# Performance work log

Hardware: AMD Instinct MI355X
Metric: run time of the kernel (lower is better)

## Reference

```python
import jax, jax.numpy as jnp
import numpy as np

IN_F, RED, WID, CLS, T = 700, 256, 4096, 20, 100


def _q4(W):
    # per-tensor symmetric INT4 STE: value is quantized, grad is identity
    scale = jnp.maximum(jnp.abs(W).max() / 7.0, 1e-8)
    return W + jax.lax.stop_gradient(jnp.round(W / scale) * scale - W)


def setup_inputs() -> dict:
    key = jax.random.key(0)
    ks = jax.random.split(key, 12)
    B = 64
    x = jax.random.normal(ks[0], (B, T, IN_F), dtype=jnp.float32)
    latent = jax.random.uniform(ks[1], (T,), dtype=jnp.float32)
    spatial_W = jax.random.normal(ks[2], (RED, IN_F), jnp.float32) / np.sqrt(IN_F)
    spatial_b = jnp.zeros((RED,), jnp.float32)
    conv_W = jax.random.normal(ks[3], (RED, RED, 5), jnp.float32) / np.sqrt(RED * 5)
    conv_b = jnp.zeros((RED,), jnp.float32)
    fc1_W = jax.random.normal(ks[4], (WID, RED), jnp.float32) / np.sqrt(RED)
    fc1_b = jnp.zeros((WID,), jnp.float32)
    fc2_W = jax.random.normal(ks[5], (CLS, WID), jnp.float32) / np.sqrt(WID)
    fc2_b = jnp.zeros((CLS,), jnp.float32)
    gain = jnp.asarray(1.0, jnp.float32)
    return {"x": x, "latent": latent, "spatial_W": spatial_W, "spatial_b": spatial_b,
            "conv_W": conv_W, "conv_b": conv_b, "fc1_W": fc1_W, "fc1_b": fc1_b,
            "fc2_W": fc2_W, "fc2_b": fc2_b, "gain": gain}


def _compute_drive(x, latent, spatial_W, spatial_b, conv_W, conv_b, fc1_W, fc1_b, gain):
    # spatial projection (INT4 STE linear) + relu : (B,T,RED)
    xp = jax.nn.relu(jnp.einsum("btf,rf->btr", x, _q4(spatial_W)) + spatial_b)
    # temporal conv1d over T, padding=2 (same), channels RED->RED
    xc = jax.lax.conv_general_dilated(
        xp.transpose(0, 2, 1), conv_W, window_strides=(1,), padding=[(2, 2)],
        dimension_numbers=("NCH", "OIH", "NCH"))
    conv_out = jax.nn.relu(xc + conv_b[None, :, None]).transpose(0, 2, 1)  # (B,T,RED)
    spatial_act = jax.nn.softplus(jnp.einsum("btr,wr->btw", conv_out, _q4(fc1_W)) + fc1_b)
    return spatial_act * latent[None, :, None] * jnp.abs(gain)  # (B,T,WID)


def reference(x, latent, spatial_W, spatial_b, conv_W, conv_b, fc1_W, fc1_b, fc2_W, fc2_b, gain):
    drive = _compute_drive(x, latent, spatial_W, spatial_b, conv_W, conv_b, fc1_W, fc1_b, gain)
    # Poisson spike sampling with straight-through estimator, then clamp at 1
    pois = jax.random.poisson(jax.random.key(42), jax.lax.stop_gradient(drive)).astype(drive.dtype)
    spikes = drive + jax.lax.stop_gradient(pois - drive)
    spikes = jnp.minimum(spikes, 1.0)
    # decay-weighted temporal reduction over T
    decay = jnp.exp(jnp.linspace(-2.0, 0.0, T)).astype(drive.dtype)
    weighted = jnp.einsum("btw,t->bw", spikes, decay)  # (B,WID)
    # dropout in eval mode = identity
    logits = weighted @ _q4(fc2_W).T + fc2_b  # (B,CLS)
    return (logits, spikes, drive)
```

## Files before the change

### kernel.cpp

```cpp
#include <hip/hip_runtime.h>
#include <stdint.h>

#define B 64
#define T 100
#define IN_F 700
#define RED 256
#define WID 4096
#define CLS 20
#define BT (B*T)
#define NELEM (BT*WID)
#define LOGITS_OFF 0
#define SPIKES_OFF (B*CLS)
#define DRIVE_OFF (SPIKES_OFF + NELEM)

#define WS_SLOTS 0
#define WS_W2Q 16
#define WS_XP  (WS_W2Q + CLS*WID)
#define WS_CO  (WS_XP + BT*RED)
#define WS_WEIGHTED (WS_CO + BT*RED)

#define SC_WST 0
#define SC_W1T (SC_WST + IN_F*RED)
#define SC_CWT (SC_W1T + RED*WID)

__host__ __device__ __forceinline__ uint32_t rotl32(uint32_t v, int r) {
  return (v << r) | (v >> (32 - r));
}

__host__ __device__ __forceinline__ void threefry2x32(uint32_t k0, uint32_t k1,
                                                      uint32_t x0, uint32_t x1,
                                                      uint32_t& o0, uint32_t& o1) {
  uint32_t k2 = k0 ^ k1 ^ 0x1BD11BDAu;
  x0 += k0; x1 += k1;
#define TF_R(r) { x0 += x1; x1 = rotl32(x1, (r)); x1 ^= x0; }
  TF_R(13) TF_R(15) TF_R(26) TF_R(6)
  x0 += k1; x1 += k2 + 1u;
  TF_R(17) TF_R(29) TF_R(16) TF_R(24)
  x0 += k2; x1 += k0 + 2u;
  TF_R(13) TF_R(15) TF_R(26) TF_R(6)
  x0 += k0; x1 += k1 + 3u;
  TF_R(17) TF_R(29) TF_R(16) TF_R(24)
  x0 += k1; x1 += k2 + 4u;
  TF_R(13) TF_R(15) TF_R(26) TF_R(6)
  x0 += k2; x1 += k0 + 5u;
#undef TF_R
  o0 = x0; o1 = x1;
}

__global__ void absmax_kernel(const float* __restrict__ w, int n, uint32_t* slot) {
  __shared__ uint32_t sm[256];
  uint32_t m = 0u;
  for (int i = blockIdx.x * 256 + threadIdx.x; i < n; i += gridDim.x * 256)
    m = max(m, __float_as_uint(fabsf(w[i])));
  sm[threadIdx.x] = m;
  __syncthreads();
  for (int s = 128; s > 0; s >>= 1) {
    if (threadIdx.x < s) sm[threadIdx.x] = max(sm[threadIdx.x], sm[threadIdx.x + s]);
    __syncthreads();
  }
  if (threadIdx.x == 0) atomicMax(slot, sm[0]);
}

__global__ void quant_t_kernel(const float* __restrict__ w, float* __restrict__ qT,
                               int Nn, int Kk, const uint32_t* __restrict__ slot) {
  float s = fmaxf(__uint_as_float(*slot) / 7.0f, 1e-8f);
  int id = blockIdx.x * 256 + threadIdx.x;
  if (id < Nn * Kk) {
    int n = id / Kk, k = id - n * Kk;
    qT[(size_t)k * Nn + n] = rintf(w[id] / s) * s;
  }
}

__global__ void quant_kernel(const float* __restrict__ w, float* __restrict__ q,
                             int n, const uint32_t* __restrict__ slot) {
  float s = fmaxf(__uint_as_float(*slot) / 7.0f, 1e-8f);
  int i = blockIdx.x * 256 + threadIdx.x;
  if (i < n) q[i] = rintf(w[i] / s) * s;
}

__global__ void convw_t_kernel(const float* __restrict__ w, float* __restrict__ wt) {
  int id = blockIdx.x * 256 + threadIdx.x;
  if (id < 256 * 1280) {
    int o = id / 1280, r = id - o * 1280;
    int ic = r / 5, h = r - ic * 5;
    wt[(size_t)((h << 8) + ic) * 256 + o] = w[id];
  }
}

template<int SRCA>
__global__ __launch_bounds__(256, 8)
void gemm32_kernel(const float* __restrict__ A, const float* __restrict__ Bt,
                   const float* __restrict__ bias, float* __restrict__ C,
                   int M, int N, int K) {
  constexpr int MT = 32, NT = 64, TM = 2, TN = 4;
  constexpr int ASR = MT + 4, BSR = NT + 4;
  __shared__ float As[32 * ASR];
  __shared__ float Bs[32 * BSR];
  int tid = threadIdx.x;
  int tx = tid & 15, ty = tid >> 4;
  int m0 = blockIdx.x * MT, n0 = blockIdx.y * NT;
  int am = tid >> 3, ak4 = (tid & 7) << 2;
  float acc[TM * TN];
#pragma unroll
  for (int i = 0; i < TM * TN; ++i) acc[i] = 0.f;

  for (int kt = 0; kt < K; kt += 32) {
    int klen = K - kt; if (klen > 32) klen = 32;
    {
      float4 av = make_float4(0.f, 0.f, 0.f, 0.f);
      if (ak4 < klen) {
        if (SRCA == 0) {
          av = *(const float4*)&A[(size_t)(m0 + am) * K + kt + ak4];
        } else {
          int k = kt + ak4;
          int h = k >> 8, ic = k & 255;
          int bt = m0 + am;
          int b = bt / T, t = bt - b * T;
          int tt = t + h - 2;
          if (tt >= 0 && tt < T)
            av = *(const float4*)&A[((size_t)(b * T + tt)) * RED + ic];
        }
      }
      As[(ak4 + 0) * ASR + am] = av.x;
      As[(ak4 + 1) * ASR + am] = av.y;
      As[(ak4 + 2) * ASR + am] = av.z;
      As[(ak4 + 3) * ASR + am] = av.w;
    }
#pragma unroll
    for (int rep = 0; rep < 2; ++rep) {
      int e = rep * 256 + tid;
      int n4 = (e & 15) << 2, kk = e >> 4;
      float4 v = make_float4(0.f, 0.f, 0.f, 0.f);
      if (kk < klen) v = *(const float4*)&Bt[(size_t)(kt + kk) * N + n0 + n4];
      *(float4*)&Bs[kk * BSR + n4] = v;
    }
    __syncthreads();
    if (klen == 32) {
#pragma unroll
      for (int kk = 0; kk < 32; ++kk) {
        float a[TM], b[TN];
#pragma unroll
        for (int i = 0; i < TM; ++i) a[i] = As[kk * ASR + ty * TM + i];
#pragma unroll
        for (int d = 0; d < TN; ++d) b[d] = Bs[kk * BSR + tx * TN + d];
#pragma unroll
        for (int j = 0; j < TM; ++j)
#pragma unroll
          for (int d = 0; d < TN; ++d)
            acc[j * TN + d] = fmaf(a[j], b[d], acc[j * TN + d]);
      }
    } else {
      for (int kk = 0; kk < klen; ++kk) {
        float a[TM], b[TN];
#pragma unroll
        for (int i = 0; i < TM; ++i) a[i] = As[kk * ASR + ty * TM + i];
#pragma unroll
        for (int d = 0; d < TN; ++d) b[d] = Bs[kk * BSR + tx * TN + d];
#pragma unroll
        for (int j = 0; j < TM; ++j)
#pragma unroll
          for (int d = 0; d < TN; ++d)
            acc[j * TN + d] = fmaf(a[j], b[d], acc[j * TN + d]);
      }
    }
    __syncthreads();
  }

  float bv[TN];
#pragma unroll
  for (int d = 0; d < TN; ++d) bv[d] = bias[n0 + tx * TN + d];
#pragma unroll
  for (int j = 0; j < TM; ++j) {
    int m = m0 + ty * TM + j;
#pragma unroll
    for (int d = 0; d < TN; ++d)
      C[(size_t)m * N + n0 + tx * TN + d] = fmaxf(acc[j * TN + d] + bv[d], 0.0f);
  }
}

__global__ __launch_bounds__(256, 4)
void fc1_kernel(const float* __restrict__ A, const float* __restrict__ Bt,
                const float* __restrict__ bias, const float* __restrict__ latent,
                const float* __restrict__ gain, float* __restrict__ C,
                int K, int N) {
  constexpr int ASR = 132, BSR = 132;
  __shared__ float As[32 * ASR];
  __shared__ float Bs[32 * BSR];
  int tid = threadIdx.x;
  int tx = tid & 15, ty = tid >> 4;
  int wid = (blockIdx.x & 7) * 200 + (blockIdx.x >> 3);
  int bx = wid % 50, by = wid / 50;
  int m0 = bx * 128, n0 = by * 128;
  float2 acc2[32];
#pragma unroll
  for (int i = 0; i < 32; ++i) acc2[i] = make_float2(0.f, 0.f);

  for (int kt = 0; kt < K; kt += 32) {
#pragma unroll
    for (int rep = 0; rep < 4; ++rep) {
      int e = rep * 256 + tid;
      int k4 = (e & 7) << 2, m = e >> 3;
      const float4 v = *(const float4*)&A[(size_t)(m0 + m) * K + kt + k4];
      As[(k4 + 0) * ASR + m] = v.x;
      As[(k4 + 1) * ASR + m] = v.y;
      As[(k4 + 2) * ASR + m] = v.z;
      As[(k4 + 3) * ASR + m] = v.w;
    }
#pragma unroll
    for (int rep = 0; rep < 4; ++rep) {
      int e = rep * 256 + tid;
      int n4 = (e & 31) << 2, kk = e >> 5;
      float4 v = *(const float4*)&Bt[(size_t)(kt + kk) * N + n0 + n4];
      *(float4*)&Bs[kk * BSR + n4] = v;
    }
    __syncthreads();
#pragma unroll
    for (int kk = 0; kk < 32; ++kk) {
      float a[8];
#pragma unroll
      for (int i = 0; i < 8; ++i) a[i] = As[kk * ASR + ty * 8 + i];
      float2 b0 = *(const float2*)&Bs[kk * BSR + tx * 4];
      float2 b1 = *(const float2*)&Bs[kk * BSR + tx * 4 + 2];
      float2 b2 = *(const float2*)&Bs[kk * BSR + 64 + tx * 4];
      float2 b3 = *(const float2*)&Bs[kk * BSR + 64 + tx * 4 + 2];
#pragma unroll
      for (int j = 0; j < 8; ++j) {
        acc2[j * 4 + 0].x = fmaf(a[j], b0.x, acc2[j * 4 + 0].x);
        acc2[j * 4 + 0].y = fmaf(a[j], b0.y, acc2[j * 4 + 0].y);
        acc2[j * 4 + 1].x = fmaf(a[j], b1.x, acc2[j * 4 + 1].x);
        acc2[j * 4 + 1].y = fmaf(a[j], b1.y, acc2[j * 4 + 1].y);
        acc2[j * 4 + 2].x = fmaf(a[j], b2.x, acc2[j * 4 + 2].x);
        acc2[j * 4 + 2].y = fmaf(a[j], b2.y, acc2[j * 4 + 2].y);
        acc2[j * 4 + 3].x = fmaf(a[j], b3.x, acc2[j * 4 + 3].x);
        acc2[j * 4 + 3].y = fmaf(a[j], b3.y, acc2[j * 4 + 3].y);
      }
    }
    __syncthreads();
  }

  float g = fabsf(gain[0]);
  float bv[8];
#pragma unroll
  for (int d = 0; d < 4; ++d) {
    bv[d] = bias[n0 + tx * 4 + d];
    bv[4 + d] = bias[n0 + 64 + tx * 4 + d];
  }
#pragma unroll
  for (int j = 0; j < 8; ++j) {
    int bt = m0 + ty * 8 + j;
    int q = bt / T;
    float lat = latent[bt - q * T];
    float o[8];
    o[0] = acc2[j * 4 + 0].x; o[1] = acc2[j * 4 + 0].y;
    o[2] = acc2[j * 4 + 1].x; o[3] = acc2[j * 4 + 1].y;
    o[4] = acc2[j * 4 + 2].x; o[5] = acc2[j * 4 + 2].y;
    o[6] = acc2[j * 4 + 3].x; o[7] = acc2[j * 4 + 3].y;
#pragma unroll
    for (int d = 0; d < 8; ++d) {
      float v = o[d] + bv[d];
      float e = expf(-fabsf(v));
      float l = log1pf(e);
      float sp = fmaxf(v, 0.0f) + l;
      o[d] = (sp * lat) * g;
    }
    float4 o0 = make_float4(o[0], o[1], o[2], o[3]);
    float4 o1 = make_float4(o[4], o[5], o[6], o[7]);
    *(float4*)&C[(size_t)bt * N + n0 + tx * 4] = o0;
    *(float4*)&C[(size_t)bt * N + n0 + 64 + tx * 4] = o1;
  }
}

__global__ __launch_bounds__(256) void spike_weighted_kernel(float* __restrict__ out,
                                                             float* __restrict__ wt,
                                                             uint32_t k0, uint32_t k1) {
  __shared__ float dec[128];
  int tid = threadIdx.x;
  if (tid < T) {
    float step = 2.0f / 99.0f;
    float a = step * (float)tid;
    dec[tid] = expf(a - 2.0f);
  }
  __syncthreads();
  int b = blockIdx.x >> 2;
  int w = ((blockIdx.x & 3) << 10) + (tid << 2);
  float acc0 = 0.f, acc1 = 0.f, acc2 = 0.f, acc3 = 0.f;
  for (int t = 0; t < T; ++t) {
    uint32_t p = (uint32_t)((b * T + t) * WID + w);
    float4 lam = *(const float4*)&out[DRIVE_OFF + p];
    float s[4];
#pragma unroll
    for (int i = 0; i < 4; ++i) {
      uint32_t y0, y1;
      threefry2x32(k0, k1, 0u, p + i, y0, y1);
      uint32_t bits = y0 ^ y1;
      float u = __uint_as_float((bits >> 9) | 0x3f800000u) - 1.0f;
      float lamv = (i == 0) ? lam.x : (i == 1) ? lam.y : (i == 2) ? lam.z : lam.w;
      s[i] = (lamv > 0.0f && logf(u) > -lamv) ? 1.0f : 0.0f;
    }
    *(float4*)&out[SPIKES_OFF + p] = make_float4(s[0], s[1], s[2], s[3]);
    float d = dec[t];
    acc0 = fmaf(s[0], d, acc0);
    acc1 = fmaf(s[1], d, acc1);
    acc2 = fmaf(s[2], d, acc2);
    acc3 = fmaf(s[3], d, acc3);
  }
  *(float4*)&wt[b * WID + w] = make_float4(acc0, acc1, acc2, acc3);
}

__global__ void logits_kernel(const float* __restrict__ wt,
                              const float* __restrict__ w2,
                              const float* __restrict__ b2,
                              float* __restrict__ out) {
  __shared__ float sm[256];
  int b = blockIdx.x / CLS, c = blockIdx.x - b * CLS;
  const float* wr = wt + (size_t)b * WID;
  const float* w2r = w2 + (size_t)c * WID;
  float p = 0.f;
  for (int w = threadIdx.x; w < WID; w += 256) p = fmaf(wr[w], w2r[w], p);
  sm[threadIdx.x] = p;
  __syncthreads();
  for (int s = 128; s > 0; s >>= 1) {
    if (threadIdx.x < s) sm[threadIdx.x] += sm[threadIdx.x + s];
    __syncthreads();
  }
  if (threadIdx.x == 0) out[LOGITS_OFF + blockIdx.x] = sm[0] + b2[c];
}

extern "C" void kernel_launch(void* const* d_in, const int* in_sizes, int n_in,
                              void* d_out, int out_size, void* d_ws, size_t ws_size,
                              hipStream_t stream) {
  (void)in_sizes; (void)n_in; (void)out_size; (void)ws_size;
  const float* x         = (const float*)d_in[0];
  const float* latent    = (const float*)d_in[1];
  const float* spatial_W = (const float*)d_in[2];
  const float* spatial_b = (const float*)d_in[3];
  const float* conv_W    = (const float*)d_in[4];
  const float* conv_b    = (const float*)d_in[5];
  const float* fc1_W     = (const float*)d_in[6];
  const float* fc1_b     = (const float*)d_in[7];
  const float* fc2_W     = (const float*)d_in[8];
  const float* fc2_b     = (const float*)d_in[9];
  const float* gain      = (const float*)d_in[10];
  float* out = (float*)d_out;
  uint32_t* wsu = (uint32_t*)d_ws;
  float* wsf = (float*)d_ws;
  float* S = out + SPIKES_OFF;

  uint32_t sk0, sk1;
  threefry2x32(0u, 42u, 0u, 1u, sk0, sk1);

  hipMemsetAsync(wsu + WS_SLOTS, 0, 3 * sizeof(uint32_t), stream);
  absmax_kernel<<<64, 256, 0, stream>>>(spatial_W, RED * IN_F, wsu + WS_SLOTS + 0);
  absmax_kernel<<<256, 256, 0, stream>>>(fc1_W, WID * RED, wsu + WS_SLOTS + 1);
  absmax_kernel<<<32, 256, 0, stream>>>(fc2_W, CLS * WID, wsu + WS_SLOTS + 2);

  quant_t_kernel<<<700, 256, 0, stream>>>(spatial_W, S + SC_WST, RED, IN_F, wsu + WS_SLOTS + 0);
  quant_t_kernel<<<4096, 256, 0, stream>>>(fc1_W, S + SC_W1T, WID, RED, wsu + WS_SLOTS + 1);
  quant_kernel<<<320, 256, 0, stream>>>(fc2_W, wsf + WS_W2Q, CLS * WID, wsu + WS_SLOTS + 2);
  convw_t_kernel<<<1280, 256, 0, stream>>>(conv_W, S + SC_CWT);

  gemm32_kernel<0><<<dim3(200, 4), 256, 0, stream>>>(
      x, S + SC_WST, spatial_b, wsf + WS_XP, BT, RED, IN_F);

  gemm32_kernel<1><<<dim3(200, 4), 256, 0, stream>>>(
      wsf + WS_XP, S + SC_CWT, conv_b, wsf + WS_CO, BT, RED, 1280);

  fc1_kernel<<<1600, 256, 0, stream>>>(
      wsf + WS_CO, S + SC_W1T, fc1_b, latent, gain, out + DRIVE_OFF, RED, WID);

  spike_weighted_kernel<<<B * 4, 256, 0, stream>>>(out, wsf + WS_WEIGHTED, sk0, sk1);

  logits_kernel<<<B * CLS, 256, 0, stream>>>(wsf + WS_WEIGHTED, wsf + WS_W2Q, fc2_b, out);
}
```

Baseline: 720.2 us.

## Double-buffer small GEMMs with 64-thread blocks and tile the weight-quantize transpose

The spatial and conv GEMMs move to a double-buffered kernel that prefetches the next K tile into registers while computing the current one. Each block now has 64 threads, each computing an 8x4 output micro-tile, and the results are stored as float4. The quantize-transpose kernel now goes through a 32x33 shared-memory tile so both its reads and its writes are coalesced. With only 64 threads per block and 800 blocks, the GEMMs may have low occupancy, and the heavier per-thread work could expose latency on this GPU.

```diff
diff --git a/kernel.cpp b/kernel.cpp
--- a/kernel.cpp
+++ b/kernel.cpp
@@ -61,13 +61,26 @@
   if (threadIdx.x == 0) atomicMax(slot, sm[0]);
 }
 
-__global__ void quant_t_kernel(const float* __restrict__ w, float* __restrict__ qT,
-                               int Nn, int Kk, const uint32_t* __restrict__ slot) {
+__global__ __launch_bounds__(256)
+void quant_t_kernel(const float* __restrict__ w, float* __restrict__ qT,
+                    int Nn, int Kk, const uint32_t* __restrict__ slot) {
+  __shared__ float tile[32][33];
   float s = fmaxf(__uint_as_float(*slot) / 7.0f, 1e-8f);
-  int id = blockIdx.x * 256 + threadIdx.x;
-  if (id < Nn * Kk) {
-    int n = id / Kk, k = id - n * Kk;
-    qT[(size_t)k * Nn + n] = rintf(w[id] / s) * s;
+  int tx = threadIdx.x & 31, ty = threadIdx.x >> 5;
+  int k0 = blockIdx.x * 32, n0 = blockIdx.y * 32;
+#pragma unroll
+  for (int r = 0; r < 32; r += 8) {
+    int n = n0 + ty + r, k = k0 + tx;
+    if (n < Nn && k < Kk) {
+      float v = w[(size_t)n * Kk + k];
+      tile[ty + r][tx] = rintf(v / s) * s;
+    }
+  }
+  __syncthreads();
+#pragma unroll
+  for (int r = 0; r < 32; r += 8) {
+    int k = k0 + ty + r, n = n0 + tx;
+    if (k < Kk && n < Nn) qT[(size_t)k * Nn + n] = tile[tx][ty + r];
   }
 }
 
@@ -88,93 +101,136 @@
 }
 
 template<int SRCA>
-__global__ __launch_bounds__(256, 8)
-void gemm32_kernel(const float* __restrict__ A, const float* __restrict__ Bt,
+__global__ __launch_bounds__(64, 2)
+void gemmdb_kernel(const float* __restrict__ A, const float* __restrict__ Bt,
                    const float* __restrict__ bias, float* __restrict__ C,
                    int M, int N, int K) {
-  constexpr int MT = 32, NT = 64, TM = 2, TN = 4;
-  constexpr int ASR = MT + 4, BSR = NT + 4;
-  __shared__ float As[32 * ASR];
-  __shared__ float Bs[32 * BSR];
+  constexpr int ASR = 36, BSR = 68;
+  __shared__ float As[2][32 * ASR];
+  __shared__ float Bs[2][32 * BSR];
   int tid = threadIdx.x;
   int tx = tid & 15, ty = tid >> 4;
-  int m0 = blockIdx.x * MT, n0 = blockIdx.y * NT;
+  int m0 = blockIdx.x * 32, n0 = blockIdx.y * 64;
   int am = tid >> 3, ak4 = (tid & 7) << 2;
-  float acc[TM * TN];
-#pragma unroll
-  for (int i = 0; i < TM * TN; ++i) acc[i] = 0.f;
-
-  for (int kt = 0; kt < K; kt += 32) {
-    int klen = K - kt; if (klen > 32) klen = 32;
-    {
-      float4 av = make_float4(0.f, 0.f, 0.f, 0.f);
-      if (ak4 < klen) {
-        if (SRCA == 0) {
-          av = *(const float4*)&A[(size_t)(m0 + am) * K + kt + ak4];
-        } else {
-          int k = kt + ak4;
-          int h = k >> 8, ic = k & 255;
-          int bt = m0 + am;
-          int b = bt / T, t = bt - b * T;
-          int tt = t + h - 2;
-          if (tt >= 0 && tt < T)
-            av = *(const float4*)&A[((size_t)(b * T + tt)) * RED + ic];
-        }
-      }
-      As[(ak4 + 0) * ASR + am] = av.x;
-      As[(ak4 + 1) * ASR + am] = av.y;
-      As[(ak4 + 2) * ASR + am] = av.z;
-      As[(ak4 + 3) * ASR + am] = av.w;
-    }
-#pragma unroll
-    for (int rep = 0; rep < 2; ++rep) {
-      int e = rep * 256 + tid;
-      int n4 = (e & 15) << 2, kk = e >> 4;
-      float4 v = make_float4(0.f, 0.f, 0.f, 0.f);
-      if (kk < klen) v = *(const float4*)&Bt[(size_t)(kt + kk) * N + n0 + n4];
-      *(float4*)&Bs[kk * BSR + n4] = v;
-    }
-    __syncthreads();
+  float acc[32];
+#pragma unroll
+  for (int i = 0; i < 32; ++i) acc[i] = 0.f;
+
+  float4 rA[4], rB[8];
+  int nt = (K + 31) >> 5;
+
+#define LOAD_TILE(kt_, klen_)                                                   \
+  {                                                                             \
+    int kt = (kt_), klen = (klen_);                                             \
+    _Pragma("unroll")                                                           \
+    for (int rep = 0; rep < 4; ++rep) {                                         \
+      int m = rep * 8 + am;                                                     \
+      float4 av = make_float4(0.f, 0.f, 0.f, 0.f);                              \
+      if (ak4 < klen) {                                                         \
+        if (SRCA == 0) {                                                        \
+          av = *(const float4*)&A[(size_t)(m0 + m) * K + kt + ak4];             \
+        } else {                                                                \
+          int k = kt + ak4;                                                     \
+          int h = k >> 8, ic = k & 255;                                         \
+          int bt = m0 + m;                                                      \
+          int b = bt / T, t = bt - b * T;                                       \
+          int tt = t + h - 2;                                                   \
+          if (tt >= 0 && tt < T)                                                \
+            av = *(const float4*)&A[((size_t)(b * T + tt)) * RED + ic];         \
+        }                                                                       \
+      }                                                                         \
+      rA[rep] = av;                                                             \
+    }                                                                           \
+    _Pragma("unroll")                                                           \
+    for (int rep = 0; rep < 8; ++rep) {                                         \
+      int e = rep * 64 + tid;                                                   \
+      int kk = e >> 4, n4 = (e & 15) << 2;                                      \
+      float4 v = make_float4(0.f, 0.f, 0.f, 0.f);                               \
+      if (kk < klen) v = *(const float4*)&Bt[(size_t)(kt + kk) * N + n0 + n4];  \
+      rB[rep] = v;                                                              \
+    }                                                                           \
+  }
+
+#define WRITE_TILE(buf_)                                                        \
+  {                                                                             \
+    int buf = (buf_);                                                           \
+    _Pragma("unroll")                                                           \
+    for (int rep = 0; rep < 4; ++rep) {                                         \
+      int m = rep * 8 + am;                                                     \
+      As[buf][(ak4 + 0) * ASR + m] = rA[rep].x;                                 \
+      As[buf][(ak4 + 1) * ASR + m] = rA[rep].y;                                 \
+      As[buf][(ak4 + 2) * ASR + m] = rA[rep].z;                                 \
+      As[buf][(ak4 + 3) * ASR + m] = rA[rep].w;                                 \
+    }                                                                           \
+    _Pragma("unroll")                                                           \
+    for (int rep = 0; rep < 8; ++rep) {                                         \
+      int e = rep * 64 + tid;                                                   \
+      int kk = e >> 4, n4 = (e & 15) << 2;                                      \
+      *(float4*)&Bs[buf][kk * BSR + n4] = rB[rep];                              \
+    }                                                                           \
+  }
+
+  {
+    int klen0 = K < 32 ? K : 32;
+    LOAD_TILE(0, klen0)
+    WRITE_TILE(0)
+  }
+  __syncthreads();
+
+  int cur = 0;
+  for (int it = 0; it < nt; ++it) {
+    int klen = K - it * 32; if (klen > 32) klen = 32;
+    bool has_next = (it + 1) < nt;
+    if (has_next) {
+      int ktn = (it + 1) * 32;
+      int klenn = K - ktn; if (klenn > 32) klenn = 32;
+      LOAD_TILE(ktn, klenn)
+    }
     if (klen == 32) {
 #pragma unroll
       for (int kk = 0; kk < 32; ++kk) {
-        float a[TM], b[TN];
-#pragma unroll
-        for (int i = 0; i < TM; ++i) a[i] = As[kk * ASR + ty * TM + i];
-#pragma unroll
-        for (int d = 0; d < TN; ++d) b[d] = Bs[kk * BSR + tx * TN + d];
-#pragma unroll
-        for (int j = 0; j < TM; ++j)
-#pragma unroll
-          for (int d = 0; d < TN; ++d)
-            acc[j * TN + d] = fmaf(a[j], b[d], acc[j * TN + d]);
+        float a[8], b[4];
+#pragma unroll
+        for (int i = 0; i < 8; ++i) a[i] = As[cur][kk * ASR + ty * 8 + i];
+#pragma unroll
+        for (int d = 0; d < 4; ++d) b[d] = Bs[cur][kk * BSR + tx * 4 + d];
+#pragma unroll
+        for (int j = 0; j < 8; ++j)
+#pragma unroll
+          for (int d = 0; d < 4; ++d)
+            acc[j * 4 + d] = fmaf(a[j], b[d], acc[j * 4 + d]);
       }
     } else {
       for (int kk = 0; kk < klen; ++kk) {
-        float a[TM], b[TN];
-#pragma unroll
-        for (int i = 0; i < TM; ++i) a[i] = As[kk * ASR + ty * TM + i];
-#pragma unroll
-        for (int d = 0; d < TN; ++d) b[d] = Bs[kk * BSR + tx * TN + d];
-#pragma unroll
-        for (int j = 0; j < TM; ++j)
-#pragma unroll
-          for (int d = 0; d < TN; ++d)
-            acc[j * TN + d] = fmaf(a[j], b[d], acc[j * TN + d]);
+        float a[8], b[4];
+#pragma unroll
+        for (int i = 0; i < 8; ++i) a[i] = As[cur][kk * ASR + ty * 8 + i];
+#pragma unroll
+        for (int d = 0; d < 4; ++d) b[d] = Bs[cur][kk * BSR + tx * 4 + d];
+#pragma unroll
+        for (int j = 0; j < 8; ++j)
+#pragma unroll
+          for (int d = 0; d < 4; ++d)
+            acc[j * 4 + d] = fmaf(a[j], b[d], acc[j * 4 + d]);
       }
     }
+    if (has_next) WRITE_TILE(cur ^ 1)
     __syncthreads();
-  }
-
-  float bv[TN];
-#pragma unroll
-  for (int d = 0; d < TN; ++d) bv[d] = bias[n0 + tx * TN + d];
-#pragma unroll
-  for (int j = 0; j < TM; ++j) {
-    int m = m0 + ty * TM + j;
-#pragma unroll
-    for (int d = 0; d < TN; ++d)
-      C[(size_t)m * N + n0 + tx * TN + d] = fmaxf(acc[j * TN + d] + bv[d], 0.0f);
+    cur ^= 1;
+  }
+#undef LOAD_TILE
+#undef WRITE_TILE
+
+  float bv[4];
+#pragma unroll
+  for (int d = 0; d < 4; ++d) bv[d] = bias[n0 + tx * 4 + d];
+#pragma unroll
+  for (int j = 0; j < 8; ++j) {
+    int m = m0 + ty * 8 + j;
+    float o[4];
+#pragma unroll
+    for (int d = 0; d < 4; ++d) o[d] = fmaxf(acc[j * 4 + d] + bv[d], 0.0f);
+    *(float4*)&C[(size_t)m * N + n0 + tx * 4] = make_float4(o[0], o[1], o[2], o[3]);
   }
 }
 
@@ -354,15 +410,15 @@
   absmax_kernel<<<256, 256, 0, stream>>>(fc1_W, WID * RED, wsu + WS_SLOTS + 1);
   absmax_kernel<<<32, 256, 0, stream>>>(fc2_W, CLS * WID, wsu + WS_SLOTS + 2);
 
-  quant_t_kernel<<<700, 256, 0, stream>>>(spatial_W, S + SC_WST, RED, IN_F, wsu + WS_SLOTS + 0);
-  quant_t_kernel<<<4096, 256, 0, stream>>>(fc1_W, S + SC_W1T, WID, RED, wsu + WS_SLOTS + 1);
+  quant_t_kernel<<<dim3(22, 8), 256, 0, stream>>>(spatial_W, S + SC_WST, RED, IN_F, wsu + WS_SLOTS + 0);
+  quant_t_kernel<<<dim3(8, 128), 256, 0, stream>>>(fc1_W, S + SC_W1T, WID, RED, wsu + WS_SLOTS + 1);
   quant_kernel<<<320, 256, 0, stream>>>(fc2_W, wsf + WS_W2Q, CLS * WID, wsu + WS_SLOTS + 2);
   convw_t_kernel<<<1280, 256, 0, stream>>>(conv_W, S + SC_CWT);
 
-  gemm32_kernel<0><<<dim3(200, 4), 256, 0, stream>>>(
+  gemmdb_kernel<0><<<dim3(200, 4), 64, 0, stream>>>(
       x, S + SC_WST, spatial_b, wsf + WS_XP, BT, RED, IN_F);
 
-  gemm32_kernel<1><<<dim3(200, 4), 256, 0, stream>>>(
+  gemmdb_kernel<1><<<dim3(200, 4), 64, 0, stream>>>(
       wsf + WS_XP, S + SC_CWT, conv_b, wsf + WS_CO, BT, RED, 1280);
 
   fc1_kernel<<<1600, 256, 0, stream>>>(
```

Result: slower. 810.8 us (+12.6%).

## Use 512-thread fc1 tiles and shared-memory tiled weight transpose-quantize

Applied to the files above, without the earlier changes.

The fc1 GEMM kernel goes from 256 to 512 threads per block over the same 128x128 tile, so each thread now computes an 8x4 micro-tile instead of 8x8. This halves per-thread register pressure and adds more waves to hide latency, at the cost of more LDS reads per FMA and narrower float2 output stores. The weight quantize-transpose kernel now goes through a padded 32x32 shared-memory tile, so both its global reads and writes are coalesced instead of the strided scatter writes it had before.

```diff
diff --git a/kernel.cpp b/kernel.cpp
--- a/kernel.cpp
+++ b/kernel.cpp
@@ -61,13 +61,26 @@
   if (threadIdx.x == 0) atomicMax(slot, sm[0]);
 }
 
-__global__ void quant_t_kernel(const float* __restrict__ w, float* __restrict__ qT,
-                               int Nn, int Kk, const uint32_t* __restrict__ slot) {
+__global__ __launch_bounds__(256)
+void quant_t_kernel(const float* __restrict__ w, float* __restrict__ qT,
+                    int Nn, int Kk, const uint32_t* __restrict__ slot) {
+  __shared__ float tile[32][33];
   float s = fmaxf(__uint_as_float(*slot) / 7.0f, 1e-8f);
-  int id = blockIdx.x * 256 + threadIdx.x;
-  if (id < Nn * Kk) {
-    int n = id / Kk, k = id - n * Kk;
-    qT[(size_t)k * Nn + n] = rintf(w[id] / s) * s;
+  int tx = threadIdx.x & 31, ty = threadIdx.x >> 5;
+  int k0 = blockIdx.x * 32, n0 = blockIdx.y * 32;
+#pragma unroll
+  for (int r = 0; r < 32; r += 8) {
+    int n = n0 + ty + r, k = k0 + tx;
+    if (n < Nn && k < Kk) {
+      float v = w[(size_t)n * Kk + k];
+      tile[ty + r][tx] = rintf(v / s) * s;
+    }
+  }
+  __syncthreads();
+#pragma unroll
+  for (int r = 0; r < 32; r += 8) {
+    int k = k0 + ty + r, n = n0 + tx;
+    if (k < Kk && n < Nn) qT[(size_t)k * Nn + n] = tile[tx][ty + r];
   }
 }
 
@@ -178,7 +191,7 @@
   }
 }
 
-__global__ __launch_bounds__(256, 4)
+__global__ __launch_bounds__(512, 4)
 void fc1_kernel(const float* __restrict__ A, const float* __restrict__ Bt,
                 const float* __restrict__ bias, const float* __restrict__ latent,
                 const float* __restrict__ gain, float* __restrict__ C,
@@ -187,18 +200,18 @@
   __shared__ float As[32 * ASR];
   __shared__ float Bs[32 * BSR];
   int tid = threadIdx.x;
-  int tx = tid & 15, ty = tid >> 4;
+  int nx = tid & 31, my = tid >> 5;
   int wid = (blockIdx.x & 7) * 200 + (blockIdx.x >> 3);
   int bx = wid % 50, by = wid / 50;
   int m0 = bx * 128, n0 = by * 128;
-  float2 acc2[32];
-#pragma unroll
-  for (int i = 0; i < 32; ++i) acc2[i] = make_float2(0.f, 0.f);
+  float acc[32];
+#pragma unroll
+  for (int i = 0; i < 32; ++i) acc[i] = 0.f;
 
   for (int kt = 0; kt < K; kt += 32) {
 #pragma unroll
-    for (int rep = 0; rep < 4; ++rep) {
-      int e = rep * 256 + tid;
+    for (int rep = 0; rep < 2; ++rep) {
+      int e = rep * 512 + tid;
       int k4 = (e & 7) << 2, m = e >> 3;
       const float4 v = *(const float4*)&A[(size_t)(m0 + m) * K + kt + k4];
       As[(k4 + 0) * ASR + m] = v.x;
@@ -207,8 +220,8 @@
       As[(k4 + 3) * ASR + m] = v.w;
     }
 #pragma unroll
-    for (int rep = 0; rep < 4; ++rep) {
-      int e = rep * 256 + tid;
+    for (int rep = 0; rep < 2; ++rep) {
+      int e = rep * 512 + tid;
       int n4 = (e & 31) << 2, kk = e >> 5;
       float4 v = *(const float4*)&Bt[(size_t)(kt + kk) * N + n0 + n4];
       *(float4*)&Bs[kk * BSR + n4] = v;
@@ -218,55 +231,41 @@
     for (int kk = 0; kk < 32; ++kk) {
       float a[8];
 #pragma unroll
-      for (int i = 0; i < 8; ++i) a[i] = As[kk * ASR + ty * 8 + i];
-      float2 b0 = *(const float2*)&Bs[kk * BSR + tx * 4];
-      float2 b1 = *(const float2*)&Bs[kk * BSR + tx * 4 + 2];
-      float2 b2 = *(const float2*)&Bs[kk * BSR + 64 + tx * 4];
-      float2 b3 = *(const float2*)&Bs[kk * BSR + 64 + tx * 4 + 2];
-#pragma unroll
-      for (int j = 0; j < 8; ++j) {
-        acc2[j * 4 + 0].x = fmaf(a[j], b0.x, acc2[j * 4 + 0].x);
-        acc2[j * 4 + 0].y = fmaf(a[j], b0.y, acc2[j * 4 + 0].y);
-        acc2[j * 4 + 1].x = fmaf(a[j], b1.x, acc2[j * 4 + 1].x);
-        acc2[j * 4 + 1].y = fmaf(a[j], b1.y, acc2[j * 4 + 1].y);
-        acc2[j * 4 + 2].x = fmaf(a[j], b2.x, acc2[j * 4 + 2].x);
-        acc2[j * 4 + 2].y = fmaf(a[j], b2.y, acc2[j * 4 + 2].y);
-        acc2[j * 4 + 3].x = fmaf(a[j], b3.x, acc2[j * 4 + 3].x);
-        acc2[j * 4 + 3].y = fmaf(a[j], b3.y, acc2[j * 4 + 3].y);
-      }
+      for (int i = 0; i < 8; ++i) a[i] = As[kk * ASR + my * 8 + i];
+      float2 b0 = *(const float2*)&Bs[kk * BSR + nx * 2];
+      float2 b1 = *(const float2*)&Bs[kk * BSR + 64 + nx * 2];
+      float b[4] = {b0.x, b0.y, b1.x, b1.y};
+#pragma unroll
+      for (int j = 0; j < 8; ++j)
+#pragma unroll
+        for (int d = 0; d < 4; ++d)
+          acc[j * 4 + d] = fmaf(a[j], b[d], acc[j * 4 + d]);
     }
     __syncthreads();
   }
 
   float g = fabsf(gain[0]);
-  float bv[8];
-#pragma unroll
-  for (int d = 0; d < 4; ++d) {
-    bv[d] = bias[n0 + tx * 4 + d];
-    bv[4 + d] = bias[n0 + 64 + tx * 4 + d];
-  }
+  float bv[4];
+  bv[0] = bias[n0 + nx * 2];
+  bv[1] = bias[n0 + nx * 2 + 1];
+  bv[2] = bias[n0 + 64 + nx * 2];
+  bv[3] = bias[n0 + 64 + nx * 2 + 1];
 #pragma unroll
   for (int j = 0; j < 8; ++j) {
-    int bt = m0 + ty * 8 + j;
+    int bt = m0 + my * 8 + j;
     int q = bt / T;
     float lat = latent[bt - q * T];
-    float o[8];
-    o[0] = acc2[j * 4 + 0].x; o[1] = acc2[j * 4 + 0].y;
-    o[2] = acc2[j * 4 + 1].x; o[3] = acc2[j * 4 + 1].y;
-    o[4] = acc2[j * 4 + 2].x; o[5] = acc2[j * 4 + 2].y;
-    o[6] = acc2[j * 4 + 3].x; o[7] = acc2[j * 4 + 3].y;
-#pragma unroll
-    for (int d = 0; d < 8; ++d) {
-      float v = o[d] + bv[d];
+    float o[4];
+#pragma unroll
+    for (int d = 0; d < 4; ++d) {
+      float v = acc[j * 4 + d] + bv[d];
       float e = expf(-fabsf(v));
       float l = log1pf(e);
       float sp = fmaxf(v, 0.0f) + l;
       o[d] = (sp * lat) * g;
     }
-    float4 o0 = make_float4(o[0], o[1], o[2], o[3]);
-    float4 o1 = make_float4(o[4], o[5], o[6], o[7]);
-    *(float4*)&C[(size_t)bt * N + n0 + tx * 4] = o0;
-    *(float4*)&C[(size_t)bt * N + n0 + 64 + tx * 4] = o1;
+    *(float2*)&C[(size_t)bt * N + n0 + nx * 2] = make_float2(o[0], o[1]);
+    *(float2*)&C[(size_t)bt * N + n0 + 64 + nx * 2] = make_float2(o[2], o[3]);
   }
 }
 
@@ -354,8 +353,8 @@
   absmax_kernel<<<256, 256, 0, stream>>>(fc1_W, WID * RED, wsu + WS_SLOTS + 1);
   absmax_kernel<<<32, 256, 0, stream>>>(fc2_W, CLS * WID, wsu + WS_SLOTS + 2);
 
-  quant_t_kernel<<<700, 256, 0, stream>>>(spatial_W, S + SC_WST, RED, IN_F, wsu + WS_SLOTS + 0);
-  quant_t_kernel<<<4096, 256, 0, stream>>>(fc1_W, S + SC_W1T, WID, RED, wsu + WS_SLOTS + 1);
+  quant_t_kernel<<<dim3(22, 8), 256, 0, stream>>>(spatial_W, S + SC_WST, RED, IN_F, wsu + WS_SLOTS + 0);
+  quant_t_kernel<<<dim3(8, 128), 256, 0, stream>>>(fc1_W, S + SC_W1T, WID, RED, wsu + WS_SLOTS + 1);
   quant_kernel<<<320, 256, 0, stream>>>(fc2_W, wsf + WS_W2Q, CLS * WID, wsu + WS_SLOTS + 2);
   convw_t_kernel<<<1280, 256, 0, stream>>>(conv_W, S + SC_CWT);
 
@@ -365,7 +364,7 @@
   gemm32_kernel<1><<<dim3(200, 4), 256, 0, stream>>>(
       wsf + WS_XP, S + SC_CWT, conv_b, wsf + WS_CO, BT, RED, 1280);
 
-  fc1_kernel<<<1600, 256, 0, stream>>>(
+  fc1_kernel<<<1600, 512, 0, stream>>>(
       wsf + WS_CO, S + SC_W1T, fc1_b, latent, gain, out + DRIVE_OFF, RED, WID);
 
   spike_weighted_kernel<<<B * 4, 256, 0, stream>>>(out, wsf + WS_WEIGHTED, sk0, sk1);
```

After: 720.1 us. About the same (-0.0%).

## Use shared-memory tiled transpose for weight quantization and 128-thread GEMM with 4x4 microtiles

Applied to the files above, without the earlier changes.

The weight quantize-transpose kernels now stage 32x32 tiles through padded shared memory, so both reads and writes are coalesced instead of issuing strided scattered stores. The spatial and conv GEMMs now run with 128 threads per 32x64 tile, each thread computing a 4x4 microtile. Shared-memory operands are read as float4 and results are written as float4. This gives each thread more arithmetic per shared load at the cost of fewer threads per block and more registers per thread.

```diff
diff --git a/kernel.cpp b/kernel.cpp
--- a/kernel.cpp
+++ b/kernel.cpp
@@ -61,13 +61,26 @@
   if (threadIdx.x == 0) atomicMax(slot, sm[0]);
 }
 
-__global__ void quant_t_kernel(const float* __restrict__ w, float* __restrict__ qT,
-                               int Nn, int Kk, const uint32_t* __restrict__ slot) {
+__global__ __launch_bounds__(256)
+void quant_t_kernel(const float* __restrict__ w, float* __restrict__ qT,
+                    int Nn, int Kk, const uint32_t* __restrict__ slot) {
+  __shared__ float tile[32][33];
   float s = fmaxf(__uint_as_float(*slot) / 7.0f, 1e-8f);
-  int id = blockIdx.x * 256 + threadIdx.x;
-  if (id < Nn * Kk) {
-    int n = id / Kk, k = id - n * Kk;
-    qT[(size_t)k * Nn + n] = rintf(w[id] / s) * s;
+  int tx = threadIdx.x & 31, ty = threadIdx.x >> 5;
+  int k0 = blockIdx.x * 32, n0 = blockIdx.y * 32;
+#pragma unroll
+  for (int r = 0; r < 32; r += 8) {
+    int n = n0 + ty + r, k = k0 + tx;
+    if (n < Nn && k < Kk) {
+      float v = w[(size_t)n * Kk + k];
+      tile[ty + r][tx] = rintf(v / s) * s;
+    }
+  }
+  __syncthreads();
+#pragma unroll
+  for (int r = 0; r < 32; r += 8) {
+    int k = k0 + ty + r, n = n0 + tx;
+    if (k < Kk && n < Nn) qT[(size_t)k * Nn + n] = tile[tx][ty + r];
   }
 }
 
@@ -88,25 +101,27 @@
 }
 
 template<int SRCA>
-__global__ __launch_bounds__(256, 8)
-void gemm32_kernel(const float* __restrict__ A, const float* __restrict__ Bt,
-                   const float* __restrict__ bias, float* __restrict__ C,
-                   int M, int N, int K) {
-  constexpr int MT = 32, NT = 64, TM = 2, TN = 4;
+__global__ __launch_bounds__(128, 8)
+void gemm128_kernel(const float* __restrict__ A, const float* __restrict__ Bt,
+                    const float* __restrict__ bias, float* __restrict__ C,
+                    int M, int N, int K) {
+  constexpr int MT = 32, NT = 64, TM = 4, TN = 4;
   constexpr int ASR = MT + 4, BSR = NT + 4;
   __shared__ float As[32 * ASR];
   __shared__ float Bs[32 * BSR];
   int tid = threadIdx.x;
   int tx = tid & 15, ty = tid >> 4;
   int m0 = blockIdx.x * MT, n0 = blockIdx.y * NT;
-  int am = tid >> 3, ak4 = (tid & 7) << 2;
   float acc[TM * TN];
 #pragma unroll
   for (int i = 0; i < TM * TN; ++i) acc[i] = 0.f;
 
   for (int kt = 0; kt < K; kt += 32) {
     int klen = K - kt; if (klen > 32) klen = 32;
-    {
+#pragma unroll
+    for (int rep = 0; rep < 2; ++rep) {
+      int e = rep * 128 + tid;
+      int am = e >> 3, ak4 = (e & 7) << 2;
       float4 av = make_float4(0.f, 0.f, 0.f, 0.f);
       if (ak4 < klen) {
         if (SRCA == 0) {
@@ -127,9 +142,9 @@
       As[(ak4 + 3) * ASR + am] = av.w;
     }
 #pragma unroll
-    for (int rep = 0; rep < 2; ++rep) {
-      int e = rep * 256 + tid;
-      int n4 = (e & 15) << 2, kk = e >> 4;
+    for (int rep = 0; rep < 4; ++rep) {
+      int e = rep * 128 + tid;
+      int kk = e >> 4, n4 = (e & 15) << 2;
       float4 v = make_float4(0.f, 0.f, 0.f, 0.f);
       if (kk < klen) v = *(const float4*)&Bt[(size_t)(kt + kk) * N + n0 + n4];
       *(float4*)&Bs[kk * BSR + n4] = v;
@@ -138,11 +153,10 @@
     if (klen == 32) {
 #pragma unroll
       for (int kk = 0; kk < 32; ++kk) {
-        float a[TM], b[TN];
-#pragma unroll
-        for (int i = 0; i < TM; ++i) a[i] = As[kk * ASR + ty * TM + i];
-#pragma unroll
-        for (int d = 0; d < TN; ++d) b[d] = Bs[kk * BSR + tx * TN + d];
+        float4 av = *(const float4*)&As[kk * ASR + ty * TM];
+        float4 bv = *(const float4*)&Bs[kk * BSR + tx * TN];
+        float a[TM] = {av.x, av.y, av.z, av.w};
+        float b[TN] = {bv.x, bv.y, bv.z, bv.w};
 #pragma unroll
         for (int j = 0; j < TM; ++j)
 #pragma unroll
@@ -151,11 +165,10 @@
       }
     } else {
       for (int kk = 0; kk < klen; ++kk) {
-        float a[TM], b[TN];
-#pragma unroll
-        for (int i = 0; i < TM; ++i) a[i] = As[kk * ASR + ty * TM + i];
-#pragma unroll
-        for (int d = 0; d < TN; ++d) b[d] = Bs[kk * BSR + tx * TN + d];
+        float4 av = *(const float4*)&As[kk * ASR + ty * TM];
+        float4 bv = *(const float4*)&Bs[kk * BSR + tx * TN];
+        float a[TM] = {av.x, av.y, av.z, av.w};
+        float b[TN] = {bv.x, bv.y, bv.z, bv.w};
 #pragma unroll
         for (int j = 0; j < TM; ++j)
 #pragma unroll
@@ -172,9 +185,10 @@
 #pragma unroll
   for (int j = 0; j < TM; ++j) {
     int m = m0 + ty * TM + j;
-#pragma unroll
-    for (int d = 0; d < TN; ++d)
-      C[(size_t)m * N + n0 + tx * TN + d] = fmaxf(acc[j * TN + d] + bv[d], 0.0f);
+    float o[TN];
+#pragma unroll
+    for (int d = 0; d < TN; ++d) o[d] = fmaxf(acc[j * TN + d] + bv[d], 0.0f);
+    *(float4*)&C[(size_t)m * N + n0 + tx * TN] = make_float4(o[0], o[1], o[2], o[3]);
   }
 }
 
@@ -354,15 +368,15 @@
   absmax_kernel<<<256, 256, 0, stream>>>(fc1_W, WID * RED, wsu + WS_SLOTS + 1);
   absmax_kernel<<<32, 256, 0, stream>>>(fc2_W, CLS * WID, wsu + WS_SLOTS + 2);
 
-  quant_t_kernel<<<700, 256, 0, stream>>>(spatial_W, S + SC_WST, RED, IN_F, wsu + WS_SLOTS + 0);
-  quant_t_kernel<<<4096, 256, 0, stream>>>(fc1_W, S + SC_W1T, WID, RED, wsu + WS_SLOTS + 1);
+  quant_t_kernel<<<dim3(22, 8), 256, 0, stream>>>(spatial_W, S + SC_WST, RED, IN_F, wsu + WS_SLOTS + 0);
+  quant_t_kernel<<<dim3(8, 128), 256, 0, stream>>>(fc1_W, S + SC_W1T, WID, RED, wsu + WS_SLOTS + 1);
   quant_kernel<<<320, 256, 0, stream>>>(fc2_W, wsf + WS_W2Q, CLS * WID, wsu + WS_SLOTS + 2);
   convw_t_kernel<<<1280, 256, 0, stream>>>(conv_W, S + SC_CWT);
 
-  gemm32_kernel<0><<<dim3(200, 4), 256, 0, stream>>>(
+  gemm128_kernel<0><<<dim3(200, 4), 128, 0, stream>>>(
       x, S + SC_WST, spatial_b, wsf + WS_XP, BT, RED, IN_F);
 
-  gemm32_kernel<1><<<dim3(200, 4), 256, 0, stream>>>(
+  gemm128_kernel<1><<<dim3(200, 4), 128, 0, stream>>>(
       wsf + WS_XP, S + SC_CWT, conv_b, wsf + WS_CO, BT, RED, 1280);
 
   fc1_kernel<<<1600, 256, 0, stream>>>(
```

Result: no change. 728.6 us (+1.2%).
